# Performance work log

Hardware: AMD Instinct MI355X
Metric: run time of the kernel (lower is better)

## Reference

```python
import jax, jax.numpy as jnp
import numpy as np

NUM_STEPS = 10  # fixed-step Dopri5 over [0, T], dt = T/NUM_STEPS (dt0=0.1, T=1.0 in source)
B, D, H = 8192, 64, 256


def setup_inputs() -> dict:
    key = jax.random.key(0)
    ks = jax.random.split(key, 4)
    x = jax.random.normal(ks[0], (B, D), jnp.float32)
    logdet_init = jnp.zeros((B,), jnp.float32)

    def lin(k, out_dim, in_dim):
        kw, kb = jax.random.split(k)
        lim = 1.0 / np.sqrt(in_dim)
        W = jax.random.uniform(kw, (out_dim, in_dim), jnp.float32, -lim, lim)
        b = jax.random.uniform(kb, (out_dim,), jnp.float32, -lim, lim)
        return W, b

    W1, b1 = lin(ks[1], H, D)
    W2, b2 = lin(ks[2], H, H)
    W3, b3 = lin(ks[3], D, H)
    T = jnp.array(1.0, jnp.float32)
    return dict(x=x, logdet_init=logdet_init, W1=W1, b1=b1, W2=W2, b2=b2, W3=W3, b3=b3, T=T)


def reference(x, logdet_init, W1, b1, W2, b2, W3, b3, T):
    # odefunc: softplus MLP, per-sample (eqx Linear semantics: W @ y + b)
    def mlp(y):  # y: (D,)
        h = jax.nn.softplus(W1 @ y + b1)
        h = jax.nn.softplus(W2 @ h + b2)
        return W3 @ h + b3

    trace_fn = jax.vmap(lambda y: jnp.trace(jax.jacfwd(mlp)(y)))  # exact trace, [B]

    def dyn(y):  # y: [B, D] -> (dy/dt [B,D], dlogdet/dt [B])
        h = jax.nn.softplus(y @ W1.T + b1)
        h = jax.nn.softplus(h @ W2.T + b2)
        dy = h @ W3.T + b3
        return dy, trace_fn(y)

    dt = T / NUM_STEPS
    # Dormand-Prince 5(4) tableau (6 stages used for the 5th-order update)
    a21 = 1/5
    a31, a32 = 3/40, 9/40
    a41, a42, a43 = 44/45, -56/15, 32/9
    a51, a52, a53, a54 = 19372/6561, -25360/2187, 64448/6561, -212/729
    a61, a62, a63, a64, a65 = 9017/3168, -355/33, 46732/5247, 49/176, -5103/18656
    c1, c3, c4, c5, c6 = 35/384, 500/1113, 125/192, -2187/6784, 11/84

    def step(carry, _):
        y, ld = carry
        k1y, k1l = dyn(y)
        k2y, k2l = dyn(y + dt * (a21 * k1y))
        k3y, k3l = dyn(y + dt * (a31 * k1y + a32 * k2y))
        k4y, k4l = dyn(y + dt * (a41 * k1y + a42 * k2y + a43 * k3y))
        k5y, k5l = dyn(y + dt * (a51 * k1y + a52 * k2y + a53 * k3y + a54 * k4y))
        k6y, k6l = dyn(y + dt * (a61 * k1y + a62 * k2y + a63 * k3y + a64 * k4y + a65 * k5y))
        y_new = y + dt * (c1 * k1y + c3 * k3y + c4 * k4y + c5 * k5y + c6 * k6y)
        ld_new = ld + dt * (c1 * k1l + c3 * k3l + c4 * k4l + c5 * k5l + c6 * k6l)
        return (y_new, ld_new), None

    (y_f, ld_f), _ = jax.lax.scan(step, (x, logdet_init), None, length=NUM_STEPS)
    return (y_f, ld_f)
```

## Files before the change

kernel.cpp:

```cpp
#include <hip/hip_runtime.h>

typedef __attribute__((ext_vector_type(4))) float f32x4;
typedef __attribute__((ext_vector_type(8))) short bf16x8;
typedef __attribute__((ext_vector_type(4))) short bf16x4;

#define MFMA16(a, b, c) __builtin_amdgcn_mfma_f32_16x16x32_bf16(a, b, c, 0, 0, 0)

#define W1F_OFF 0
#define W2F_OFF 16384
#define CF_OFF  81920
#define W3F_OFF 147456

__device__ __forceinline__ short f2bf(float f) {
  __bf16 b = (__bf16)f;
  return __builtin_bit_cast(short, b);
}

__device__ __forceinline__ void sp_sig(float z, float& h, float& s) {
  float a = fabsf(z);
#if __has_builtin(__builtin_amdgcn_exp2f)
  float t = __builtin_amdgcn_exp2f(a * -1.44269504f);
#else
  float t = __expf(-a);
#endif
  float o = 1.f + t;
#if __has_builtin(__builtin_amdgcn_rcpf)
  float r = __builtin_amdgcn_rcpf(o);
#else
  float r = 1.f / o;
#endif
#if __has_builtin(__builtin_amdgcn_logf)
  float l2 = __builtin_amdgcn_logf(o);
#else
  float l2 = __logf(o) * 1.44269504f;
#endif
  h = fmaxf(z, 0.f) + 0.69314718f * l2;
  s = (z >= 0.f) ? r : 1.f - r;
}

__global__ __launch_bounds__(512) void cnf_prep(const float* __restrict__ W1,
                                                const float* __restrict__ W2,
                                                const float* __restrict__ W3,
                                                short* __restrict__ ws) {
  int e = blockIdx.x * 512 + threadIdx.x;
  int j = e & 7;
  int l = (e >> 3) & 63;
  int g = l >> 4, lm = l & 15;
  float val;
  if (e < 16384) {
    int t = e >> 9, kt = t & 1, mt = t >> 1;
    val = W1[(mt * 16 + lm) * 64 + kt * 32 + g * 8 + j];
  } else if (e < 81920) {
    int t = (e - 16384) >> 9, kt = t & 7, mt = t >> 3;
    val = W2[(mt * 16 + lm) * 256 + kt * 32 + g * 8 + j];
  } else if (e < 147456) {
    int t = (e - 81920) >> 9, kt = t & 7, mt = t >> 3;
    int m = mt * 16 + lm, k = kt * 32 + g * 8 + j;
    float a2 = 0.f;
#pragma unroll 16
    for (int d = 0; d < 64; ++d) a2 += W1[k * 64 + d] * W3[d * 256 + m];
    val = W2[m * 256 + k] * a2;
  } else {
    int t = (e - 147456) >> 9, kt = t & 7, mt = t >> 3;
    val = W3[(mt * 16 + lm) * 256 + kt * 32 + g * 8 + j];
  }
  ws[e] = f2bf(val);
}

__global__ __launch_bounds__(512) void cnf_main(
    const float* __restrict__ x, const float* __restrict__ ld_init,
    const float* __restrict__ b1g, const float* __restrict__ b2g,
    const float* __restrict__ b3g, const float* __restrict__ Tg,
    const short* __restrict__ ws, float* __restrict__ outy,
    float* __restrict__ outl) {
  __shared__ __align__(16) short w1f[16384];
  __shared__ __align__(16) short w3f[16384];
  __shared__ __align__(16) short ytL[32 * 88];
  __shared__ __align__(16) short h1L[32 * 264];
  __shared__ __align__(16) short s1L_[32 * 264];
  __shared__ __align__(16) short h2L[32 * 264];
  __shared__ __align__(16) float dyL[32 * 68];
  __shared__ __align__(16) float trPT[32][12];

  const int tid = threadIdx.x;
  const int lane = tid & 63, wv = tid >> 6;
  const int sl = tid >> 4, q = tid & 15;
  const int lg = lane >> 4, lm = lane & 15;
  const int ko8 = lg << 3;

  {
    const f32x4* s1p = (const f32x4*)(ws + W1F_OFF);
    f32x4* d1 = (f32x4*)w1f;
#pragma unroll
    for (int i = 0; i < 4; ++i) d1[tid + 512 * i] = s1p[tid + 512 * i];
    const f32x4* s3p = (const f32x4*)(ws + W3F_OFF);
    f32x4* d3 = (f32x4*)w3f;
#pragma unroll
    for (int i = 0; i < 4; ++i) d3[tid + 512 * i] = s3p[tid + 512 * i];
  }

  const int row0a = (2 * wv + 0) * 16 + (lg << 2);
  const int row0b = (2 * wv + 1) * 16 + (lg << 2);
  const f32x4 bias1a = *(const f32x4*)&b1g[row0a];
  const f32x4 bias1b = *(const f32x4*)&b1g[row0b];
  const f32x4 bias2a = *(const f32x4*)&b2g[row0a];
  const f32x4 bias2b = *(const f32x4*)&b2g[row0b];
  const int m3 = wv & 3, c3 = wv >> 2;
  const f32x4 bias3 = *(const f32x4*)&b3g[m3 * 16 + (lg << 2)];

  const bf16x8* w2fG = (const bf16x8*)(ws + W2F_OFF);
  const bf16x8* cfG  = (const bf16x8*)(ws + CF_OFF);

  const int sg = blockIdx.x * 32 + sl;
  f32x4 y = *(const f32x4*)&x[sg * 64 + q * 4];
  float ld = ld_init[sg];
  const float dt = Tg[0] * 0.1f;

  __syncthreads();

  auto dyn = [&](f32x4 yin, f32x4& dy, float& tr)
      __attribute__((always_inline)) {
    bf16x4 yb;
#pragma unroll
    for (int r = 0; r < 4; ++r) yb[r] = f2bf(yin[r]);
    *(bf16x4*)&ytL[sl * 88 + q * 4] = yb;
    __syncthreads();

    f32x4 a00 = bias1a, a01 = bias1a, a10 = bias1b, a11 = bias1b;
#pragma unroll
    for (int kt = 0; kt < 2; ++kt) {
      bf16x8 A0 = *(const bf16x8*)&w1f[(((2 * wv + 0) * 2 + kt) * 64 + lane) * 8];
      bf16x8 A1 = *(const bf16x8*)&w1f[(((2 * wv + 1) * 2 + kt) * 64 + lane) * 8];
      bf16x8 B0 = *(const bf16x8*)&ytL[lm * 88 + kt * 32 + ko8];
      bf16x8 B1 = *(const bf16x8*)&ytL[(16 + lm) * 88 + kt * 32 + ko8];
      a00 = MFMA16(A0, B0, a00); a01 = MFMA16(A0, B1, a01);
      a10 = MFMA16(A1, B0, a10); a11 = MFMA16(A1, B1, a11);
    }
    {
      auto epi1 = [&](const f32x4& z4, int r0, int c)
          __attribute__((always_inline)) {
        int sc = c * 16 + lm;
        bf16x4 hh, ss;
#pragma unroll
        for (int r = 0; r < 4; ++r) {
          float h, s;
          sp_sig(z4[r], h, s);
          hh[r] = f2bf(h); ss[r] = f2bf(s);
        }
        *(bf16x4*)&h1L[sc * 264 + r0] = hh;
        *(bf16x4*)&s1L_[sc * 264 + r0] = ss;
      };
      epi1(a00, row0a, 0); epi1(a01, row0a, 1);
      epi1(a10, row0b, 0); epi1(a11, row0b, 1);
    }
    __syncthreads();

    f32x4 c00 = bias2a, c01 = bias2a, c10 = bias2b, c11 = bias2b;
#pragma unroll
    for (int kt = 0; kt < 8; ++kt) {
      bf16x8 A0 = w2fG[((2 * wv + 0) * 8 + kt) * 64 + lane];
      bf16x8 A1 = w2fG[((2 * wv + 1) * 8 + kt) * 64 + lane];
      bf16x8 B0 = *(const bf16x8*)&h1L[lm * 264 + kt * 32 + ko8];
      bf16x8 B1 = *(const bf16x8*)&h1L[(16 + lm) * 264 + kt * 32 + ko8];
      c00 = MFMA16(A0, B0, c00); c01 = MFMA16(A0, B1, c01);
      c10 = MFMA16(A1, B0, c10); c11 = MFMA16(A1, B1, c11);
    }
    f32x4 s200, s201, s210, s211;
    {
      auto epi2 = [&](const f32x4& z4, int r0, int c, f32x4& s2o)
          __attribute__((always_inline)) {
        int sc = c * 16 + lm;
        bf16x4 hh;
#pragma unroll
        for (int r = 0; r < 4; ++r) {
          float h, s;
          sp_sig(z4[r], h, s);
          hh[r] = f2bf(h); s2o[r] = s;
        }
        *(bf16x4*)&h2L[sc * 264 + r0] = hh;
      };
      epi2(c00, row0a, 0, s200); epi2(c01, row0a, 1, s201);
      epi2(c10, row0b, 0, s210); epi2(c11, row0b, 1, s211);
    }

    f32x4 u00 = {0,0,0,0}, u01 = {0,0,0,0}, u10 = {0,0,0,0}, u11 = {0,0,0,0};
#pragma unroll
    for (int kt = 0; kt < 8; ++kt) {
      bf16x8 A0 = cfG[((2 * wv + 0) * 8 + kt) * 64 + lane];
      bf16x8 A1 = cfG[((2 * wv + 1) * 8 + kt) * 64 + lane];
      bf16x8 B0 = *(const bf16x8*)&s1L_[lm * 264 + kt * 32 + ko8];
      bf16x8 B1 = *(const bf16x8*)&s1L_[(16 + lm) * 264 + kt * 32 + ko8];
      u00 = MFMA16(A0, B0, u00); u01 = MFMA16(A0, B1, u01);
      u10 = MFMA16(A1, B0, u10); u11 = MFMA16(A1, B1, u11);
    }
    float pl0 = 0.f, pl1 = 0.f;
#pragma unroll
    for (int r = 0; r < 4; ++r) {
      pl0 += u00[r] * s200[r] + u10[r] * s210[r];
      pl1 += u01[r] * s201[r] + u11[r] * s211[r];
    }
    pl0 += __shfl_xor(pl0, 16); pl0 += __shfl_xor(pl0, 32);
    pl1 += __shfl_xor(pl1, 16); pl1 += __shfl_xor(pl1, 32);
    if (lane < 16) { trPT[lane][wv] = pl0; trPT[16 + lane][wv] = pl1; }

    f32x4 d3a = bias3;
#pragma unroll
    for (int kt = 0; kt < 8; ++kt) {
      bf16x8 A0 = *(const bf16x8*)&w3f[((m3 * 8 + kt) * 64 + lane) * 8];
      bf16x8 B0 = *(const bf16x8*)&h2L[(c3 * 16 + lm) * 264 + kt * 32 + ko8];
      d3a = MFMA16(A0, B0, d3a);
    }
    *(f32x4*)&dyL[(c3 * 16 + lm) * 68 + m3 * 16 + (lg << 2)] = d3a;
    __syncthreads();

    dy = *(const f32x4*)&dyL[sl * 68 + q * 4];
    f32x4 t0 = *(const f32x4*)&trPT[sl][0];
    f32x4 t1 = *(const f32x4*)&trPT[sl][4];
    f32x4 ts = t0 + t1;
    tr = ts[0] + ts[1] + ts[2] + ts[3];
  };

  const float A21 = dt * (1.f / 5.f);
  const float A31 = dt * (3.f / 40.f), A32 = dt * (9.f / 40.f);
  const float A41 = dt * (44.f / 45.f), A42 = dt * (-56.f / 15.f),
              A43 = dt * (32.f / 9.f);
  const float A51 = dt * (19372.f / 6561.f), A52 = dt * (-25360.f / 2187.f),
              A53 = dt * (64448.f / 6561.f), A54 = dt * (-212.f / 729.f);
  const float A61 = dt * (9017.f / 3168.f), A62 = dt * (-355.f / 33.f),
              A63 = dt * (46732.f / 5247.f), A64 = dt * (49.f / 176.f),
              A65 = dt * (-5103.f / 18656.f);
  const float C1 = dt * (35.f / 384.f), C3 = dt * (500.f / 1113.f),
              C4 = dt * (125.f / 192.f), C5 = dt * (-2187.f / 6784.f),
              C6 = dt * (11.f / 84.f);

  f32x4 k1, k2, k3, k4, k5, k6;
  float tr;
#pragma unroll 1
  for (int step = 0; step < 10; ++step) {
    dyn(y, k1, tr);                                          ld += C1 * tr;
    dyn(y + A21 * k1, k2, tr);
    dyn(y + A31 * k1 + A32 * k2, k3, tr);                    ld += C3 * tr;
    dyn(y + A41 * k1 + A42 * k2 + A43 * k3, k4, tr);         ld += C4 * tr;
    dyn(y + A51 * k1 + A52 * k2 + A53 * k3 + A54 * k4, k5, tr);
    ld += C5 * tr;
    dyn(y + A61 * k1 + A62 * k2 + A63 * k3 + A64 * k4 + A65 * k5, k6, tr);
    ld += C6 * tr;
    y = y + C1 * k1 + C3 * k3 + C4 * k4 + C5 * k5 + C6 * k6;
  }

  *(f32x4*)&outy[sg * 64 + q * 4] = y;
  if (q == 0) outl[sg] = ld;
}

extern "C" void kernel_launch(void* const* d_in, const int* in_sizes, int n_in,
                              void* d_out, int out_size, void* d_ws, size_t ws_size,
                              hipStream_t stream) {
  const float* x  = (const float*)d_in[0];
  const float* l0 = (const float*)d_in[1];
  const float* W1 = (const float*)d_in[2];
  const float* b1 = (const float*)d_in[3];
  const float* W2 = (const float*)d_in[4];
  const float* b2 = (const float*)d_in[5];
  const float* W3 = (const float*)d_in[6];
  const float* b3 = (const float*)d_in[7];
  const float* Tp = (const float*)d_in[8];
  short* ws = (short*)d_ws;

  cnf_prep<<<dim3(320), dim3(512), 0, stream>>>(W1, W2, W3, ws);

  float* outy = (float*)d_out;
  float* outl = outy + 8192 * 64;
  cnf_main<<<dim3(256), dim3(512), 0, stream>>>(x, l0, b1, b2, b3, Tp, ws,
                                                outy, outl);
}
```

Measured before the change: 380.7 us.

## Read W1/W3 fragments from global instead of LDS and stage biases in LDS

Removes the 64KB of LDS holding W1 and W3 fragments and instead loads those MFMA A-operands straight from global memory (L2-cached), as was already done for W2 and the trace coefficient matrix. Biases move from per-thread registers into small LDS arrays and are added in the epilogues instead of seeding the accumulators. The aim is to shrink LDS and register footprint so more blocks fit per CU. The cost is extra global/L2 traffic on every stage evaluation and an added barrier before the W3 GEMM for the trace partials.

```diff
diff --git a/kernel.cpp b/kernel.cpp
--- a/kernel.cpp
+++ b/kernel.cpp
@@ -73,14 +73,13 @@
     const float* __restrict__ b3g, const float* __restrict__ Tg,
     const short* __restrict__ ws, float* __restrict__ outy,
     float* __restrict__ outl) {
-  __shared__ __align__(16) short w1f[16384];
-  __shared__ __align__(16) short w3f[16384];
   __shared__ __align__(16) short ytL[32 * 88];
   __shared__ __align__(16) short h1L[32 * 264];
   __shared__ __align__(16) short s1L_[32 * 264];
   __shared__ __align__(16) short h2L[32 * 264];
   __shared__ __align__(16) float dyL[32 * 68];
-  __shared__ __align__(16) float trPT[32][12];
+  __shared__ float trP[8][32];
+  __shared__ float b1L[256], b2L[256], b3L[64];
 
   const int tid = threadIdx.x;
   const int lane = tid & 63, wv = tid >> 6;
@@ -88,28 +87,13 @@
   const int lg = lane >> 4, lm = lane & 15;
   const int ko8 = lg << 3;
 
-  {
-    const f32x4* s1p = (const f32x4*)(ws + W1F_OFF);
-    f32x4* d1 = (f32x4*)w1f;
-#pragma unroll
-    for (int i = 0; i < 4; ++i) d1[tid + 512 * i] = s1p[tid + 512 * i];
-    const f32x4* s3p = (const f32x4*)(ws + W3F_OFF);
-    f32x4* d3 = (f32x4*)w3f;
-#pragma unroll
-    for (int i = 0; i < 4; ++i) d3[tid + 512 * i] = s3p[tid + 512 * i];
-  }
-
-  const int row0a = (2 * wv + 0) * 16 + (lg << 2);
-  const int row0b = (2 * wv + 1) * 16 + (lg << 2);
-  const f32x4 bias1a = *(const f32x4*)&b1g[row0a];
-  const f32x4 bias1b = *(const f32x4*)&b1g[row0b];
-  const f32x4 bias2a = *(const f32x4*)&b2g[row0a];
-  const f32x4 bias2b = *(const f32x4*)&b2g[row0b];
-  const int m3 = wv & 3, c3 = wv >> 2;
-  const f32x4 bias3 = *(const f32x4*)&b3g[m3 * 16 + (lg << 2)];
-
+  if (tid < 256) { b1L[tid] = b1g[tid]; b2L[tid] = b2g[tid]; }
+  else if (tid < 320) b3L[tid - 256] = b3g[tid - 256];
+
+  const bf16x8* w1fG = (const bf16x8*)(ws + W1F_OFF);
   const bf16x8* w2fG = (const bf16x8*)(ws + W2F_OFF);
   const bf16x8* cfG  = (const bf16x8*)(ws + CF_OFF);
+  const bf16x8* w3fG = (const bf16x8*)(ws + W3F_OFF);
 
   const int sg = blockIdx.x * 32 + sl;
   f32x4 y = *(const f32x4*)&x[sg * 64 + q * 4];
@@ -126,36 +110,36 @@
     *(bf16x4*)&ytL[sl * 88 + q * 4] = yb;
     __syncthreads();
 
-    f32x4 a00 = bias1a, a01 = bias1a, a10 = bias1b, a11 = bias1b;
+    f32x4 a00 = {0,0,0,0}, a01 = {0,0,0,0}, a10 = {0,0,0,0}, a11 = {0,0,0,0};
 #pragma unroll
     for (int kt = 0; kt < 2; ++kt) {
-      bf16x8 A0 = *(const bf16x8*)&w1f[(((2 * wv + 0) * 2 + kt) * 64 + lane) * 8];
-      bf16x8 A1 = *(const bf16x8*)&w1f[(((2 * wv + 1) * 2 + kt) * 64 + lane) * 8];
+      bf16x8 A0 = w1fG[((2 * wv + 0) * 2 + kt) * 64 + lane];
+      bf16x8 A1 = w1fG[((2 * wv + 1) * 2 + kt) * 64 + lane];
       bf16x8 B0 = *(const bf16x8*)&ytL[lm * 88 + kt * 32 + ko8];
       bf16x8 B1 = *(const bf16x8*)&ytL[(16 + lm) * 88 + kt * 32 + ko8];
       a00 = MFMA16(A0, B0, a00); a01 = MFMA16(A0, B1, a01);
       a10 = MFMA16(A1, B0, a10); a11 = MFMA16(A1, B1, a11);
     }
     {
-      auto epi1 = [&](const f32x4& z4, int r0, int c)
+      auto epi1 = [&](const f32x4& z4, int r2, int c)
           __attribute__((always_inline)) {
+        int row0 = (2 * wv + r2) * 16 + (lg << 2);
         int sc = c * 16 + lm;
         bf16x4 hh, ss;
 #pragma unroll
         for (int r = 0; r < 4; ++r) {
           float h, s;
-          sp_sig(z4[r], h, s);
+          sp_sig(z4[r] + b1L[row0 + r], h, s);
           hh[r] = f2bf(h); ss[r] = f2bf(s);
         }
-        *(bf16x4*)&h1L[sc * 264 + r0] = hh;
-        *(bf16x4*)&s1L_[sc * 264 + r0] = ss;
+        *(bf16x4*)&h1L[sc * 264 + row0] = hh;
+        *(bf16x4*)&s1L_[sc * 264 + row0] = ss;
       };
-      epi1(a00, row0a, 0); epi1(a01, row0a, 1);
-      epi1(a10, row0b, 0); epi1(a11, row0b, 1);
-    }
-    __syncthreads();
-
-    f32x4 c00 = bias2a, c01 = bias2a, c10 = bias2b, c11 = bias2b;
+      epi1(a00, 0, 0); epi1(a01, 0, 1); epi1(a10, 1, 0); epi1(a11, 1, 1);
+    }
+    __syncthreads();
+
+    f32x4 c00 = {0,0,0,0}, c01 = {0,0,0,0}, c10 = {0,0,0,0}, c11 = {0,0,0,0};
 #pragma unroll
     for (int kt = 0; kt < 8; ++kt) {
       bf16x8 A0 = w2fG[((2 * wv + 0) * 8 + kt) * 64 + lane];
@@ -167,20 +151,21 @@
     }
     f32x4 s200, s201, s210, s211;
     {
-      auto epi2 = [&](const f32x4& z4, int r0, int c, f32x4& s2o)
+      auto epi2 = [&](const f32x4& z4, int r2, int c, f32x4& s2o)
           __attribute__((always_inline)) {
+        int row0 = (2 * wv + r2) * 16 + (lg << 2);
         int sc = c * 16 + lm;
         bf16x4 hh;
 #pragma unroll
         for (int r = 0; r < 4; ++r) {
           float h, s;
-          sp_sig(z4[r], h, s);
+          sp_sig(z4[r] + b2L[row0 + r], h, s);
           hh[r] = f2bf(h); s2o[r] = s;
         }
-        *(bf16x4*)&h2L[sc * 264 + r0] = hh;
+        *(bf16x4*)&h2L[sc * 264 + row0] = hh;
       };
-      epi2(c00, row0a, 0, s200); epi2(c01, row0a, 1, s201);
-      epi2(c10, row0b, 0, s210); epi2(c11, row0b, 1, s211);
+      epi2(c00, 0, 0, s200); epi2(c01, 0, 1, s201);
+      epi2(c10, 1, 0, s210); epi2(c11, 1, 1, s211);
     }
 
     f32x4 u00 = {0,0,0,0}, u01 = {0,0,0,0}, u10 = {0,0,0,0}, u11 = {0,0,0,0};
@@ -201,23 +186,32 @@
     }
     pl0 += __shfl_xor(pl0, 16); pl0 += __shfl_xor(pl0, 32);
     pl1 += __shfl_xor(pl1, 16); pl1 += __shfl_xor(pl1, 32);
-    if (lane < 16) { trPT[lane][wv] = pl0; trPT[16 + lane][wv] = pl1; }
-
-    f32x4 d3a = bias3;
+    if (lane < 16) { trP[wv][lane] = pl0; trP[wv][16 + lane] = pl1; }
+    __syncthreads();
+
+    f32x4 d3a = {0,0,0,0};
+    const int m3 = wv & 3, c3 = wv >> 2;
 #pragma unroll
     for (int kt = 0; kt < 8; ++kt) {
-      bf16x8 A0 = *(const bf16x8*)&w3f[((m3 * 8 + kt) * 64 + lane) * 8];
+      bf16x8 A0 = w3fG[(m3 * 8 + kt) * 64 + lane];
       bf16x8 B0 = *(const bf16x8*)&h2L[(c3 * 16 + lm) * 264 + kt * 32 + ko8];
       d3a = MFMA16(A0, B0, d3a);
     }
-    *(f32x4*)&dyL[(c3 * 16 + lm) * 68 + m3 * 16 + (lg << 2)] = d3a;
+    {
+      int d0r = m3 * 16 + (lg << 2);
+      int sc = c3 * 16 + lm;
+      f32x4 dv;
+#pragma unroll
+      for (int r = 0; r < 4; ++r) dv[r] = d3a[r] + b3L[d0r + r];
+      *(f32x4*)&dyL[sc * 68 + d0r] = dv;
+    }
     __syncthreads();
 
     dy = *(const f32x4*)&dyL[sl * 68 + q * 4];
-    f32x4 t0 = *(const f32x4*)&trPT[sl][0];
-    f32x4 t1 = *(const f32x4*)&trPT[sl][4];
-    f32x4 ts = t0 + t1;
-    tr = ts[0] + ts[1] + ts[2] + ts[3];
+    float t = 0.f;
+#pragma unroll
+    for (int w = 0; w < 8; ++w) t += trP[w][sl];
+    tr = t;
   };
 
   const float A21 = dt * (1.f / 5.f);
```

Result: slower. 469.4 us (+23.3%).
